# Performance work log

Measured on AMD Instinct MI355X. Metric: run time of the kernel, lower is better.

Reference implementation:

```python
import jax, jax.numpy as jnp
import numpy as np

N = 50000
E = 800000
IN_DIM = 128
HIDDEN = 32
HEADS = 4
OUT_DIM = 64
NEG_SLOPE = 0.2


def _glorot(key, shape):
    fan_in, fan_out = shape[0], shape[-1]
    lim = jnp.sqrt(6.0 / (fan_in + fan_out))
    return jax.random.uniform(key, shape, jnp.float32, -lim, lim)


def setup_inputs() -> dict:
    key = jax.random.key(0)
    ks = jax.random.split(key, 16)
    x = jax.random.normal(ks[0], (N, IN_DIM), jnp.float32)
    edge_index = jax.random.randint(ks[1], (2, E), 0, N, jnp.int64)
    # layer 0: in_dim -> hidden, heads, concat
    W1 = _glorot(ks[2], (IN_DIM, HEADS * HIDDEN))
    a_src1 = _glorot(ks[3], (HEADS, HIDDEN))
    a_dst1 = _glorot(ks[4], (HEADS, HIDDEN))
    b1 = jnp.zeros((HEADS * HIDDEN,), jnp.float32)
    # layer 1: hidden*heads -> hidden, heads, concat
    W2 = _glorot(ks[5], (HEADS * HIDDEN, HEADS * HIDDEN))
    a_src2 = _glorot(ks[6], (HEADS, HIDDEN))
    a_dst2 = _glorot(ks[7], (HEADS, HIDDEN))
    b2 = jnp.zeros((HEADS * HIDDEN,), jnp.float32)
    # layer 2: hidden*heads -> out_dim, heads, concat=False (mean over heads)
    W3 = _glorot(ks[8], (HEADS * HIDDEN, HEADS * OUT_DIM))
    a_src3 = _glorot(ks[9], (HEADS, OUT_DIM))
    a_dst3 = _glorot(ks[10], (HEADS, OUT_DIM))
    b3 = jnp.zeros((OUT_DIM,), jnp.float32)
    return {"x": x, "edge_index": edge_index,
            "W1": W1, "a_src1": a_src1, "a_dst1": a_dst1, "b1": b1,
            "W2": W2, "a_src2": a_src2, "a_dst2": a_dst2, "b2": b2,
            "W3": W3, "a_src3": a_src3, "a_dst3": a_dst3, "b3": b3}


def gat_conv(x, src, dst, W, a_src, a_dst, bias, out_ch, concat):
    # linear projection, per-head view: [N, H, C]
    h = (x @ W).reshape(N, HEADS, out_ch)
    # per-node attention logits, gathered to edges: [E, H]
    alpha_src = jnp.einsum('nhc,hc->nh', h, a_src)
    alpha_dst = jnp.einsum('nhc,hc->nh', h, a_dst)
    e = jax.nn.leaky_relu(alpha_src[src] + alpha_dst[dst], NEG_SLOPE)
    # segment softmax over incoming edges of each dst node
    m = jax.ops.segment_max(e, dst, num_segments=N)  # [N, H]
    m = jnp.where(jnp.isfinite(m), m, 0.0)
    p = jnp.exp(e - m[dst])  # [E, H]
    denom = jax.ops.segment_sum(p, dst, num_segments=N)  # [N, H]
    alpha = p / (denom[dst] + 1e-16)
    # weighted scatter-add of source features: [N, H, C]
    out = jax.ops.segment_sum(h[src] * alpha[:, :, None], dst, num_segments=N)
    if concat:
        return out.reshape(N, HEADS * out_ch) + bias
    return out.mean(axis=1) + bias


def reference(x, edge_index, W1, a_src1, a_dst1, b1, W2, a_src2, a_dst2, b2,
              W3, a_src3, a_dst3, b3):
    src, dst = edge_index[0], edge_index[1]
    x = gat_conv(x, src, dst, W1, a_src1, a_dst1, b1, HIDDEN, True)
    x = gat_conv(x, src, dst, W2, a_src2, a_dst2, b2, HIDDEN, True)
    x = gat_conv(x, src, dst, W3, a_src3, a_dst3, b3, OUT_DIM, False)
    return x
```

## Files before the change

### kernel.cpp

```cpp
#include <hip/hip_runtime.h>
#include <hip/hip_fp16.h>
#include <math.h>

#define NNODES 50000
#define NEDGES 800000

typedef _Float16 half8 __attribute__((ext_vector_type(8)));
typedef float floatx4 __attribute__((ext_vector_type(4)));


__global__ void zero_i32(int* __restrict__ p, int n) {
    int i = blockIdx.x * 256 + threadIdx.x;
    if (i < n) p[i] = 0;
}

__global__ void hist_kernel(const int* __restrict__ dst, int* __restrict__ counts, int e) {
    int i = blockIdx.x * 256 + threadIdx.x;
    if (i < e) atomicAdd(&counts[dst[i]], 1);
}

__global__ void scan1_kernel(const int* __restrict__ counts, int* __restrict__ row_ptr,
                             int* __restrict__ bsums, int n) {
    __shared__ int s[256];
    int tid = threadIdx.x;
    int i = blockIdx.x * 256 + tid;
    int v = (i < n) ? counts[i] : 0;
    s[tid] = v;
    __syncthreads();
    #pragma unroll
    for (int o = 1; o < 256; o <<= 1) {
        int t = (tid >= o) ? s[tid - o] : 0;
        __syncthreads();
        s[tid] += t;
        __syncthreads();
    }
    if (i < n) row_ptr[i + 1] = s[tid];
    if (tid == 255) bsums[blockIdx.x] = s[255];
}

__global__ void scan2_kernel(int* __restrict__ bsums, int nb) {
    __shared__ int s[256];
    int tid = threadIdx.x;
    int v = (tid < nb) ? bsums[tid] : 0;
    s[tid] = v;
    __syncthreads();
    #pragma unroll
    for (int o = 1; o < 256; o <<= 1) {
        int t = (tid >= o) ? s[tid - o] : 0;
        __syncthreads();
        s[tid] += t;
        __syncthreads();
    }
    if (tid < nb) bsums[tid] = s[tid] - v;
}

__global__ void scan3_kernel(int* __restrict__ row_ptr, const int* __restrict__ bsums,
                             int* __restrict__ cursor, int n) {
    int i = blockIdx.x * 256 + threadIdx.x;
    if (i < n) {
        row_ptr[i + 1] += bsums[blockIdx.x];
        cursor[i] = 0;
    }
    if (i == 0) row_ptr[0] = 0;
}

__global__ void fill_kernel(const int* __restrict__ src, const int* __restrict__ dst,
                            const int* __restrict__ row_ptr, int* __restrict__ cursor,
                            int* __restrict__ csr_src, int e) {
    int i = blockIdx.x * 256 + threadIdx.x;
    if (i < e) {
        int d = dst[i];
        int pos = atomicAdd(&cursor[d], 1);
        csr_src[row_ptr[d] + pos] = src[i];
    }
}

__global__ void prep_v_kernel(const float* __restrict__ W3, const float* __restrict__ as3,
                              const float* __restrict__ ad3, float* __restrict__ Vs,
                              float* __restrict__ Vd) {
    int id = blockIdx.x * 256 + threadIdx.x;
    if (id >= 1024) return;
    int which = id >> 9;
    int rem = id & 511;
    int k = rem >> 2;
    int hd = rem & 3;
    const float* av = which ? ad3 : as3;
    float s = 0.f;
    #pragma unroll 8
    for (int c = 0; c < 64; ++c)
        s += W3[(size_t)k * 256 + hd * 64 + c] * av[hd * 64 + c];
    (which ? Vd : Vs)[hd * 128 + k] = s;
}

__global__ void prep_wr_kernel(const float* __restrict__ W3, __half* __restrict__ Wr) {
    int id = blockIdx.x * 256 + threadIdx.x;
    if (id >= 64 * 512) return;
    int c = id >> 9;
    int rem = id & 511;
    int hd = rem >> 7;
    int k = rem & 127;
    Wr[(size_t)c * 512 + hd * 128 + k] = __float2half(W3[(size_t)k * 256 + hd * 64 + c]);
}

__global__ __launch_bounds__(256) void alpha3_kernel(const __half* __restrict__ A,
                                                     const float* __restrict__ Vs,
                                                     const float* __restrict__ Vd,
                                                     float* __restrict__ asrc,
                                                     float* __restrict__ adst, int n) {
    int wid = threadIdx.x >> 6;
    int lane = threadIdx.x & 63;
    int node = blockIdx.x * 4 + wid;
    if (node >= n) return;
    unsigned raw = *(const unsigned*)(A + (size_t)node * 128 + lane * 2);
    float2 f = __half22float2(*(const __half2*)&raw);
    float ss[4], sd[4];
    #pragma unroll
    for (int hd = 0; hd < 4; ++hd) {
        ss[hd] = f.x * Vs[hd * 128 + lane * 2] + f.y * Vs[hd * 128 + lane * 2 + 1];
        sd[hd] = f.x * Vd[hd * 128 + lane * 2] + f.y * Vd[hd * 128 + lane * 2 + 1];
    }
    #pragma unroll
    for (int o = 1; o < 64; o <<= 1) {
        #pragma unroll
        for (int hd = 0; hd < 4; ++hd) {
            ss[hd] += __shfl_xor(ss[hd], o);
            sd[hd] += __shfl_xor(sd[hd], o);
        }
    }
    if (lane == 0) {
        #pragma unroll
        for (int hd = 0; hd < 4; ++hd) {
            asrc[(size_t)node * 4 + hd] = ss[hd];
            adst[(size_t)node * 4 + hd] = sd[hd];
        }
    }
}


template <bool AF32, int LAYER>
__global__ __launch_bounds__(256, 3) void gemm_mfma(const void* __restrict__ A_,
                                                    const float* __restrict__ Wf,
                                                    const float* __restrict__ a_src,
                                                    const float* __restrict__ a_dst,
                                                    __half* __restrict__ H,
                                                    float* __restrict__ asrc,
                                                    float* __restrict__ adst, int n) {
    const int M = 128, CH = 32;
    __shared__ __half As[128][136];
    __shared__ __half Ws[64][136];
    int tid = threadIdx.x;
    int row0 = blockIdx.x * 128;
    int col0 = blockIdx.y * 64;

    if constexpr (AF32) {
        const float* Af = (const float*)A_;
        #pragma unroll
        for (int it = 0; it < 8; ++it) {
            int flat = tid + it * 256;
            int r = flat >> 4;
            int kq = (flat & 15) * 8;
            int gr = row0 + r;
            float4 v0 = {0.f, 0.f, 0.f, 0.f}, v1 = {0.f, 0.f, 0.f, 0.f};
            if (gr < n) {
                v0 = *(const float4*)&Af[(size_t)gr * 128 + kq];
                v1 = *(const float4*)&Af[(size_t)gr * 128 + kq + 4];
            }
            __half2 h0 = __floats2half2_rn(v0.x, v0.y);
            __half2 h1 = __floats2half2_rn(v0.z, v0.w);
            __half2 h2 = __floats2half2_rn(v1.x, v1.y);
            __half2 h3 = __floats2half2_rn(v1.z, v1.w);
            uint4 st = {*(unsigned*)&h0, *(unsigned*)&h1, *(unsigned*)&h2, *(unsigned*)&h3};
            *(uint4*)&As[r][kq] = st;
        }
    } else {
        const __half* Ah = (const __half*)A_;
        #pragma unroll
        for (int it = 0; it < 8; ++it) {
            int flat = tid + it * 256;
            int r = flat >> 4;
            int kq = (flat & 15) * 8;
            int gr = row0 + r;
            float4 v = {0.f, 0.f, 0.f, 0.f};
            if (gr < n) v = *(const float4*)&Ah[(size_t)gr * 128 + kq];
            *(float4*)&As[r][kq] = v;
        }
    }
    #pragma unroll
    for (int it = 0; it < 4; ++it) {
        int flat = tid + it * 256;
        int kp = flat >> 4;
        int c4 = (flat & 15) * 4;
        int k = kp * 2;
        float4 va = *(const float4*)&Wf[(size_t)k * M + col0 + c4];
        float4 vb = *(const float4*)&Wf[(size_t)(k + 1) * M + col0 + c4];
        *(__half2*)&Ws[c4 + 0][k] = __floats2half2_rn(va.x, vb.x);
        *(__half2*)&Ws[c4 + 1][k] = __floats2half2_rn(va.y, vb.y);
        *(__half2*)&Ws[c4 + 2][k] = __floats2half2_rn(va.z, vb.z);
        *(__half2*)&Ws[c4 + 3][k] = __floats2half2_rn(va.w, vb.w);
    }
    __syncthreads();

    int lane = tid & 63;
    int wid = tid >> 6;
    int wm = (wid >> 1) * 64;
    int wn = (wid & 1) * 32;
    int l15 = lane & 15;
    int l4 = lane >> 4;

    floatx4 acc[4][2];
    #pragma unroll
    for (int mf = 0; mf < 4; ++mf)
        #pragma unroll
        for (int nf = 0; nf < 2; ++nf) {
            floatx4 z = {0.f, 0.f, 0.f, 0.f};
            acc[mf][nf] = z;
        }

    #pragma unroll
    for (int ks = 0; ks < 4; ++ks) {
        int kb = ks * 32 + l4 * 8;
        half8 b0 = *(const half8*)&Ws[wn + l15][kb];
        half8 b1 = *(const half8*)&Ws[wn + 16 + l15][kb];
        #pragma unroll
        for (int mf = 0; mf < 4; ++mf) {
            half8 a = *(const half8*)&As[wm + mf * 16 + l15][kb];
            acc[mf][0] = __builtin_amdgcn_mfma_f32_16x16x32_f16(a, b0, acc[mf][0], 0, 0, 0);
            acc[mf][1] = __builtin_amdgcn_mfma_f32_16x16x32_f16(a, b1, acc[mf][1], 0, 0, 0);
        }
    }

    #pragma unroll
    for (int mf = 0; mf < 4; ++mf)
        #pragma unroll
        for (int r = 0; r < 4; ++r) {
            int gr = row0 + wm + mf * 16 + l4 * 4 + r;
            if (gr < n) {
                H[(size_t)gr * M + col0 + wn + l15] = __float2half(acc[mf][0][r]);
                H[(size_t)gr * M + col0 + wn + 16 + l15] = __float2half(acc[mf][1][r]);
            }
        }

    int hw = (col0 + wn) / CH;
    float vs0 = a_src[hw * CH + l15];
    float vs1 = a_src[hw * CH + 16 + l15];
    float vd0 = a_dst[hw * CH + l15];
    float vd1 = a_dst[hw * CH + 16 + l15];

    #pragma unroll
    for (int mf = 0; mf < 4; ++mf)
        #pragma unroll
        for (int r = 0; r < 4; ++r) {
            float ss = acc[mf][0][r] * vs0 + acc[mf][1][r] * vs1;
            float sd = acc[mf][0][r] * vd0 + acc[mf][1][r] * vd1;
            #pragma unroll
            for (int o = 1; o < 16; o <<= 1) {
                ss += __shfl_xor(ss, o);
                sd += __shfl_xor(sd, o);
            }
            int gr = row0 + wm + mf * 16 + l4 * 4 + r;
            if (l15 == 0 && gr < n) {
                asrc[(size_t)gr * 4 + hw] = ss;
                adst[(size_t)gr * 4 + hw] = sd;
            }
        }
}


template <int LAYER>
__global__ __launch_bounds__(256) void aggregate_kernel(
    const __half* __restrict__ h, const float* __restrict__ asrc,
    const float* __restrict__ adst, const int* __restrict__ csr_src,
    const int* __restrict__ row_ptr, const float* __restrict__ bias,
    __half* __restrict__ out, int n) {
    __shared__ float lds[4][332];
    int wid = threadIdx.x >> 6;
    int lane = threadIdx.x & 63;
    int node = blockIdx.x * 4 + wid;
    if (node >= n) return;
    float* Wp = lds[wid];
    int* Ws = (int*)&lds[wid][264];
    int start = row_ptr[node];
    int end = row_ptr[node + 1];
    float4 ad = *(const float4*)&adst[(size_t)node * 4];

    int l32 = lane & 31, head = l32 >> 3, j_off = lane >> 5;
    int hoff = head * 66;

    float acc0 = 0.f, acc1 = 0.f, acc2 = 0.f, acc3 = 0.f, pw = 0.f;

    for (int base = start; base < end; base += 64) {
        int cnt = end - base;
        if (cnt > 64) cnt = 64;
        int s = 0;
        float4 pv = {0.f, 0.f, 0.f, 0.f};
        if (lane < cnt) {
            s = csr_src[base + lane];
            float4 a = *(const float4*)&asrc[(size_t)s * 4];
            float e0 = a.x + ad.x; e0 = (e0 > 0.f) ? e0 : 0.2f * e0;
            float e1 = a.y + ad.y; e1 = (e1 > 0.f) ? e1 : 0.2f * e1;
            float e2 = a.z + ad.z; e2 = (e2 > 0.f) ? e2 : 0.2f * e2;
            float e3 = a.w + ad.w; e3 = (e3 > 0.f) ? e3 : 0.2f * e3;
            pv.x = __expf(e0); pv.y = __expf(e1); pv.z = __expf(e2); pv.w = __expf(e3);
        }
        Wp[0 * 66 + lane] = pv.x;
        Wp[1 * 66 + lane] = pv.y;
        Wp[2 * 66 + lane] = pv.z;
        Wp[3 * 66 + lane] = pv.w;
        Ws[lane] = s;
        __builtin_amdgcn_wave_barrier();
        asm volatile("" ::: "memory");
        for (int jj = 0; jj < cnt; jj += 16) {
            float w[8]; int sa[8];
            #pragma unroll
            for (int u = 0; u < 8; ++u) {
                int j = jj + 2 * u + j_off;
                w[u] = Wp[hoff + j];
                sa[u] = Ws[j];
            }
            float2 v[8];
            #pragma unroll
            for (int u = 0; u < 8; ++u)
                v[u] = *(const float2*)(h + (size_t)sa[u] * 128 + l32 * 4);
            #pragma unroll
            for (int u = 0; u < 8; ++u) {
                float2 f01 = __half22float2(((const __half2*)&v[u])[0]);
                float2 f23 = __half22float2(((const __half2*)&v[u])[1]);
                acc0 += w[u] * f01.x;
                acc1 += w[u] * f01.y;
                acc2 += w[u] * f23.x;
                acc3 += w[u] * f23.y;
                pw += w[u];
            }
        }
        __builtin_amdgcn_wave_barrier();
        asm volatile("" ::: "memory");
    }

    acc0 += __shfl_xor(acc0, 32);
    acc1 += __shfl_xor(acc1, 32);
    acc2 += __shfl_xor(acc2, 32);
    acc3 += __shfl_xor(acc3, 32);
    pw += __shfl_xor(pw, 32);
    if (lane < 32) {
        float inv = 1.f / (pw + 1e-16f);
        float4 b = *(const float4*)&bias[l32 * 4];
        __half2 ha = __floats2half2_rn(acc0 * inv + b.x, acc1 * inv + b.y);
        __half2 hb = __floats2half2_rn(acc2 * inv + b.z, acc3 * inv + b.w);
        uint2 st = {*(unsigned int*)&ha, *(unsigned int*)&hb};
        *(uint2*)&out[(size_t)node * 128 + l32 * 4] = st;
    }
}


__global__ __launch_bounds__(256) void aggregate_x_kernel(
    const __half* __restrict__ A, const float* __restrict__ asrc,
    const float* __restrict__ adst, const int* __restrict__ csr_src,
    const int* __restrict__ row_ptr, __half* __restrict__ S, int n) {
    __shared__ float lds[4][320];
    int wid = threadIdx.x >> 6;
    int lane = threadIdx.x & 63;
    int node = blockIdx.x * 4 + wid;
    if (node >= n) return;
    float* Wp4 = lds[wid];
    int* Ws = (int*)&lds[wid][256];
    int start = row_ptr[node];
    int end = row_ptr[node + 1];
    float4 ad = *(const float4*)&adst[(size_t)node * 4];

    float a00 = 0.f, a01 = 0.f, a10 = 0.f, a11 = 0.f;
    float a20 = 0.f, a21 = 0.f, a30 = 0.f, a31 = 0.f;
    float4 psum = {0.f, 0.f, 0.f, 0.f};

    for (int base = start; base < end; base += 64) {
        int cnt = end - base;
        if (cnt > 64) cnt = 64;
        int s = 0;
        float4 pv = {0.f, 0.f, 0.f, 0.f};
        if (lane < cnt) {
            s = csr_src[base + lane];
            float4 a = *(const float4*)&asrc[(size_t)s * 4];
            float e0 = a.x + ad.x; e0 = (e0 > 0.f) ? e0 : 0.2f * e0;
            float e1 = a.y + ad.y; e1 = (e1 > 0.f) ? e1 : 0.2f * e1;
            float e2 = a.z + ad.z; e2 = (e2 > 0.f) ? e2 : 0.2f * e2;
            float e3 = a.w + ad.w; e3 = (e3 > 0.f) ? e3 : 0.2f * e3;
            pv.x = __expf(e0); pv.y = __expf(e1); pv.z = __expf(e2); pv.w = __expf(e3);
            psum.x += pv.x; psum.y += pv.y; psum.z += pv.z; psum.w += pv.w;
        }
        *(float4*)&Wp4[lane * 4] = pv;
        Ws[lane] = s;
        __builtin_amdgcn_wave_barrier();
        asm volatile("" ::: "memory");
        for (int jj = 0; jj < cnt; jj += 8) {
            int sa[8];
            #pragma unroll
            for (int u = 0; u < 8; ++u) sa[u] = Ws[jj + u];
            unsigned raw[8];
            #pragma unroll
            for (int u = 0; u < 8; ++u)
                raw[u] = *(const unsigned*)(A + (size_t)sa[u] * 128 + lane * 2);
            #pragma unroll
            for (int u = 0; u < 8; ++u) {
                float4 p = *(const float4*)&Wp4[(jj + u) * 4];
                float2 f = __half22float2(*(const __half2*)&raw[u]);
                a00 += p.x * f.x; a01 += p.x * f.y;
                a10 += p.y * f.x; a11 += p.y * f.y;
                a20 += p.z * f.x; a21 += p.z * f.y;
                a30 += p.w * f.x; a31 += p.w * f.y;
            }
        }
        __builtin_amdgcn_wave_barrier();
        asm volatile("" ::: "memory");
    }

    #pragma unroll
    for (int o = 1; o < 64; o <<= 1) {
        psum.x += __shfl_xor(psum.x, o);
        psum.y += __shfl_xor(psum.y, o);
        psum.z += __shfl_xor(psum.z, o);
        psum.w += __shfl_xor(psum.w, o);
    }
    float s0 = 0.25f / (psum.x + 1e-16f);
    float s1 = 0.25f / (psum.y + 1e-16f);
    float s2 = 0.25f / (psum.z + 1e-16f);
    float s3 = 0.25f / (psum.w + 1e-16f);
    size_t sb = (size_t)node * 512 + lane * 2;
    *(__half2*)&S[sb + 0 * 128] = __floats2half2_rn(a00 * s0, a01 * s0);
    *(__half2*)&S[sb + 1 * 128] = __floats2half2_rn(a10 * s1, a11 * s1);
    *(__half2*)&S[sb + 2 * 128] = __floats2half2_rn(a20 * s2, a21 * s2);
    *(__half2*)&S[sb + 3 * 128] = __floats2half2_rn(a30 * s3, a31 * s3);
}


__global__ __launch_bounds__(256, 3) void post_gemm(const __half* __restrict__ S,
                                                    const __half* __restrict__ Wr,
                                                    const float* __restrict__ b3,
                                                    float* __restrict__ out, int n) {
    __shared__ __half As[128][136];
    __shared__ __half Ws[64][136];
    int tid = threadIdx.x;
    int row0 = blockIdx.x * 128;
    int lane = tid & 63;
    int wid = tid >> 6;
    int wm = (wid >> 1) * 64;
    int wn = (wid & 1) * 32;
    int l15 = lane & 15;
    int l4 = lane >> 4;

    floatx4 acc[4][2];
    #pragma unroll
    for (int mf = 0; mf < 4; ++mf)
        #pragma unroll
        for (int nf = 0; nf < 2; ++nf) {
            floatx4 z = {0.f, 0.f, 0.f, 0.f};
            acc[mf][nf] = z;
        }

    for (int kb = 0; kb < 512; kb += 128) {
        #pragma unroll
        for (int it = 0; it < 8; ++it) {
            int flat = tid + it * 256;
            int r = flat >> 4;
            int kq = (flat & 15) * 8;
            int gr = row0 + r;
            float4 v = {0.f, 0.f, 0.f, 0.f};
            if (gr < n) v = *(const float4*)&S[(size_t)gr * 512 + kb + kq];
            *(float4*)&As[r][kq] = v;
        }
        #pragma unroll
        for (int it = 0; it < 4; ++it) {
            int flat = tid + it * 256;
            int r = flat >> 4;
            int kq = (flat & 15) * 8;
            *(float4*)&Ws[r][kq] = *(const float4*)&Wr[(size_t)r * 512 + kb + kq];
        }
        __syncthreads();
        #pragma unroll
        for (int ks = 0; ks < 4; ++ks) {
            int kk = ks * 32 + l4 * 8;
            half8 b0 = *(const half8*)&Ws[wn + l15][kk];
            half8 b1 = *(const half8*)&Ws[wn + 16 + l15][kk];
            #pragma unroll
            for (int mf = 0; mf < 4; ++mf) {
                half8 a = *(const half8*)&As[wm + mf * 16 + l15][kk];
                acc[mf][0] = __builtin_amdgcn_mfma_f32_16x16x32_f16(a, b0, acc[mf][0], 0, 0, 0);
                acc[mf][1] = __builtin_amdgcn_mfma_f32_16x16x32_f16(a, b1, acc[mf][1], 0, 0, 0);
            }
        }
        __syncthreads();
    }

    float bl = b3[wn + l15];
    float bh = b3[wn + 16 + l15];
    #pragma unroll
    for (int mf = 0; mf < 4; ++mf)
        #pragma unroll
        for (int r = 0; r < 4; ++r) {
            int gr = row0 + wm + mf * 16 + l4 * 4 + r;
            if (gr < n) {
                out[(size_t)gr * 64 + wn + l15] = acc[mf][0][r] + bl;
                out[(size_t)gr * 64 + wn + 16 + l15] = acc[mf][1][r] + bh;
            }
        }
}


extern "C" void kernel_launch(void* const* d_in, const int* in_sizes, int n_in,
                              void* d_out, int out_size, void* d_ws, size_t ws_size,
                              hipStream_t stream) {
    const float* x = (const float*)d_in[0];
    const int* ei = (const int*)d_in[1];
    const int* src = ei;
    const int* dst = ei + NEDGES;
    const float* W1 = (const float*)d_in[2];
    const float* as1 = (const float*)d_in[3];
    const float* ad1 = (const float*)d_in[4];
    const float* b1 = (const float*)d_in[5];
    const float* W2 = (const float*)d_in[6];
    const float* as2 = (const float*)d_in[7];
    const float* ad2 = (const float*)d_in[8];
    const float* b2 = (const float*)d_in[9];
    const float* W3 = (const float*)d_in[10];
    const float* as3 = (const float*)d_in[11];
    const float* ad3 = (const float*)d_in[12];
    const float* b3 = (const float*)d_in[13];

    char* ws = (char*)d_ws;
    size_t off = 0;
    auto take = [&](size_t bytes) -> char* {
        char* p = ws + off;
        off = (off + bytes + 255) & ~(size_t)255;
        return p;
    };
    int* csr = (int*)take((size_t)NEDGES * 4);
    int* row_ptr = (int*)take((size_t)(NNODES + 1) * 4);
    int* counts = (int*)take((size_t)NNODES * 4);
    int* cursor = (int*)take((size_t)NNODES * 4);
    int* bsums = (int*)take(1024 * 4);
    float* asrc = (float*)take((size_t)NNODES * 4 * 4);
    float* adst = (float*)take((size_t)NNODES * 4 * 4);
    __half* hbuf = (__half*)take((size_t)NNODES * 128 * 2);
    __half* buf1h = (__half*)take((size_t)NNODES * 128 * 2);
    __half* Sbuf = (__half*)take((size_t)NNODES * 512 * 2);
    float* Vs = (float*)take(512 * 4);
    float* Vd = (float*)take(512 * 4);
    __half* Wr = (__half*)take((size_t)64 * 512 * 2);
    float* outp = (float*)d_out;

    int nbN = (NNODES + 255) / 256;
    int nbE = (NEDGES + 255) / 256;
    int gnodeAgg = (NNODES + 3) / 4;

    zero_i32<<<nbN, 256, 0, stream>>>(counts, NNODES);
    hist_kernel<<<nbE, 256, 0, stream>>>(dst, counts, NEDGES);
    scan1_kernel<<<nbN, 256, 0, stream>>>(counts, row_ptr, bsums, NNODES);
    scan2_kernel<<<1, 256, 0, stream>>>(bsums, nbN);
    scan3_kernel<<<nbN, 256, 0, stream>>>(row_ptr, bsums, cursor, NNODES);
    fill_kernel<<<nbE, 256, 0, stream>>>(src, dst, row_ptr, cursor, csr, NEDGES);
    prep_v_kernel<<<4, 256, 0, stream>>>(W3, as3, ad3, Vs, Vd);
    prep_wr_kernel<<<128, 256, 0, stream>>>(W3, Wr);

    dim3 gA((NNODES + 127) / 128, 2);

    gemm_mfma<true, 1><<<gA, 256, 0, stream>>>(x, W1, as1, ad1, hbuf, asrc, adst, NNODES);
    aggregate_kernel<1><<<gnodeAgg, 256, 0, stream>>>(hbuf, asrc, adst, csr, row_ptr, b1, buf1h, NNODES);

    gemm_mfma<false, 2><<<gA, 256, 0, stream>>>(buf1h, W2, as2, ad2, hbuf, asrc, adst, NNODES);
    aggregate_kernel<2><<<gnodeAgg, 256, 0, stream>>>(hbuf, asrc, adst, csr, row_ptr, b2, buf1h, NNODES);

    alpha3_kernel<<<gnodeAgg, 256, 0, stream>>>(buf1h, Vs, Vd, asrc, adst, NNODES);
    aggregate_x_kernel<<<gnodeAgg, 256, 0, stream>>>(buf1h, asrc, adst, csr, row_ptr, Sbuf, NNODES);
    post_gemm<<<(NNODES + 127) / 128, 256, 0, stream>>>(Sbuf, Wr, b3, outp, NNODES);
}
```

Baseline: 297.1 us.

## Fuse layer-3 attention logits into layer-2 aggregation and remap lanes per channel

Removes the separate alpha3 kernel by computing the layer-3 source and destination logits inside the layer-2 aggregation epilogue, using the freshly computed outputs still in registers. To support this, the aggregation is remapped so each of the 64 lanes owns two channels across all edges, not half the edges with four channels each. The per-edge weights are now stored as a float4 per edge in LDS, and the final cross-half shuffle reduction goes away. Separate asrc3/adst3 buffers avoid overwriting the logits still being read. The trade-off is that each edge gather is now a 4-byte load per lane instead of 8 bytes, with twice as many inner iterations per edge chunk.

```diff
diff --git a/kernel.cpp b/kernel.cpp
--- a/kernel.cpp
+++ b/kernel.cpp
@@ -102,40 +102,6 @@
     Wr[(size_t)c * 512 + hd * 128 + k] = __float2half(W3[(size_t)k * 256 + hd * 64 + c]);
 }
 
-__global__ __launch_bounds__(256) void alpha3_kernel(const __half* __restrict__ A,
-                                                     const float* __restrict__ Vs,
-                                                     const float* __restrict__ Vd,
-                                                     float* __restrict__ asrc,
-                                                     float* __restrict__ adst, int n) {
-    int wid = threadIdx.x >> 6;
-    int lane = threadIdx.x & 63;
-    int node = blockIdx.x * 4 + wid;
-    if (node >= n) return;
-    unsigned raw = *(const unsigned*)(A + (size_t)node * 128 + lane * 2);
-    float2 f = __half22float2(*(const __half2*)&raw);
-    float ss[4], sd[4];
-    #pragma unroll
-    for (int hd = 0; hd < 4; ++hd) {
-        ss[hd] = f.x * Vs[hd * 128 + lane * 2] + f.y * Vs[hd * 128 + lane * 2 + 1];
-        sd[hd] = f.x * Vd[hd * 128 + lane * 2] + f.y * Vd[hd * 128 + lane * 2 + 1];
-    }
-    #pragma unroll
-    for (int o = 1; o < 64; o <<= 1) {
-        #pragma unroll
-        for (int hd = 0; hd < 4; ++hd) {
-            ss[hd] += __shfl_xor(ss[hd], o);
-            sd[hd] += __shfl_xor(sd[hd], o);
-        }
-    }
-    if (lane == 0) {
-        #pragma unroll
-        for (int hd = 0; hd < 4; ++hd) {
-            asrc[(size_t)node * 4 + hd] = ss[hd];
-            adst[(size_t)node * 4 + hd] = sd[hd];
-        }
-    }
-}
-
 
 template <bool AF32, int LAYER>
 __global__ __launch_bounds__(256, 3) void gemm_mfma(const void* __restrict__ A_,
@@ -266,27 +232,27 @@
 }
 
 
-template <int LAYER>
+template <int LAYER, bool FUSE_A3>
 __global__ __launch_bounds__(256) void aggregate_kernel(
     const __half* __restrict__ h, const float* __restrict__ asrc,
     const float* __restrict__ adst, const int* __restrict__ csr_src,
     const int* __restrict__ row_ptr, const float* __restrict__ bias,
-    __half* __restrict__ out, int n) {
-    __shared__ float lds[4][332];
+    const float* __restrict__ Vs, const float* __restrict__ Vd,
+    __half* __restrict__ out, float* __restrict__ asrc3,
+    float* __restrict__ adst3, int n) {
+    __shared__ float lds[4][320];
     int wid = threadIdx.x >> 6;
     int lane = threadIdx.x & 63;
     int node = blockIdx.x * 4 + wid;
     if (node >= n) return;
-    float* Wp = lds[wid];
-    int* Ws = (int*)&lds[wid][264];
+    float* Wp4 = lds[wid];
+    int* Ws = (int*)&lds[wid][256];
     int start = row_ptr[node];
     int end = row_ptr[node + 1];
     float4 ad = *(const float4*)&adst[(size_t)node * 4];
-
-    int l32 = lane & 31, head = l32 >> 3, j_off = lane >> 5;
-    int hoff = head * 66;
-
-    float acc0 = 0.f, acc1 = 0.f, acc2 = 0.f, acc3 = 0.f, pw = 0.f;
+    int head = lane >> 4;
+
+    float acc0 = 0.f, acc1 = 0.f, pw = 0.f;
 
     for (int base = start; base < end; base += 64) {
         int cnt = end - base;
@@ -302,33 +268,26 @@
             float e3 = a.w + ad.w; e3 = (e3 > 0.f) ? e3 : 0.2f * e3;
             pv.x = __expf(e0); pv.y = __expf(e1); pv.z = __expf(e2); pv.w = __expf(e3);
         }
-        Wp[0 * 66 + lane] = pv.x;
-        Wp[1 * 66 + lane] = pv.y;
-        Wp[2 * 66 + lane] = pv.z;
-        Wp[3 * 66 + lane] = pv.w;
+        *(float4*)&Wp4[lane * 4] = pv;
         Ws[lane] = s;
         __builtin_amdgcn_wave_barrier();
         asm volatile("" ::: "memory");
-        for (int jj = 0; jj < cnt; jj += 16) {
+        for (int jj = 0; jj < cnt; jj += 8) {
             float w[8]; int sa[8];
             #pragma unroll
             for (int u = 0; u < 8; ++u) {
-                int j = jj + 2 * u + j_off;
-                w[u] = Wp[hoff + j];
-                sa[u] = Ws[j];
-            }
-            float2 v[8];
+                w[u] = Wp4[(jj + u) * 4 + head];
+                sa[u] = Ws[jj + u];
+            }
+            unsigned raw[8];
             #pragma unroll
             for (int u = 0; u < 8; ++u)
-                v[u] = *(const float2*)(h + (size_t)sa[u] * 128 + l32 * 4);
+                raw[u] = *(const unsigned*)(h + (size_t)sa[u] * 128 + lane * 2);
             #pragma unroll
             for (int u = 0; u < 8; ++u) {
-                float2 f01 = __half22float2(((const __half2*)&v[u])[0]);
-                float2 f23 = __half22float2(((const __half2*)&v[u])[1]);
-                acc0 += w[u] * f01.x;
-                acc1 += w[u] * f01.y;
-                acc2 += w[u] * f23.x;
-                acc3 += w[u] * f23.y;
+                float2 f = __half22float2(*(const __half2*)&raw[u]);
+                acc0 += w[u] * f.x;
+                acc1 += w[u] * f.y;
                 pw += w[u];
             }
         }
@@ -336,18 +295,31 @@
         asm volatile("" ::: "memory");
     }
 
-    acc0 += __shfl_xor(acc0, 32);
-    acc1 += __shfl_xor(acc1, 32);
-    acc2 += __shfl_xor(acc2, 32);
-    acc3 += __shfl_xor(acc3, 32);
-    pw += __shfl_xor(pw, 32);
-    if (lane < 32) {
-        float inv = 1.f / (pw + 1e-16f);
-        float4 b = *(const float4*)&bias[l32 * 4];
-        __half2 ha = __floats2half2_rn(acc0 * inv + b.x, acc1 * inv + b.y);
-        __half2 hb = __floats2half2_rn(acc2 * inv + b.z, acc3 * inv + b.w);
-        uint2 st = {*(unsigned int*)&ha, *(unsigned int*)&hb};
-        *(uint2*)&out[(size_t)node * 128 + l32 * 4] = st;
+    float inv = 1.f / (pw + 1e-16f);
+    float2 b = *(const float2*)&bias[lane * 2];
+    float o0 = acc0 * inv + b.x;
+    float o1 = acc1 * inv + b.y;
+    *(__half2*)&out[(size_t)node * 128 + lane * 2] = __floats2half2_rn(o0, o1);
+
+    if constexpr (FUSE_A3) {
+        float r[8];
+        #pragma unroll
+        for (int hd = 0; hd < 4; ++hd) {
+            r[hd]     = o0 * Vs[hd * 128 + lane * 2] + o1 * Vs[hd * 128 + lane * 2 + 1];
+            r[hd + 4] = o0 * Vd[hd * 128 + lane * 2] + o1 * Vd[hd * 128 + lane * 2 + 1];
+        }
+        #pragma unroll
+        for (int o = 1; o < 64; o <<= 1) {
+            #pragma unroll
+            for (int q = 0; q < 8; ++q) r[q] += __shfl_xor(r[q], o);
+        }
+        if (lane == 0) {
+            #pragma unroll
+            for (int hd = 0; hd < 4; ++hd) {
+                asrc3[(size_t)node * 4 + hd] = r[hd];
+                adst3[(size_t)node * 4 + hd] = r[hd + 4];
+            }
+        }
     }
 }
 
@@ -538,6 +510,8 @@
     int* bsums = (int*)take(1024 * 4);
     float* asrc = (float*)take((size_t)NNODES * 4 * 4);
     float* adst = (float*)take((size_t)NNODES * 4 * 4);
+    float* asrc3 = (float*)take((size_t)NNODES * 4 * 4);
+    float* adst3 = (float*)take((size_t)NNODES * 4 * 4);
     __half* hbuf = (__half*)take((size_t)NNODES * 128 * 2);
     __half* buf1h = (__half*)take((size_t)NNODES * 128 * 2);
     __half* Sbuf = (__half*)take((size_t)NNODES * 512 * 2);
@@ -562,12 +536,13 @@
     dim3 gA((NNODES + 127) / 128, 2);
 
     gemm_mfma<true, 1><<<gA, 256, 0, stream>>>(x, W1, as1, ad1, hbuf, asrc, adst, NNODES);
-    aggregate_kernel<1><<<gnodeAgg, 256, 0, stream>>>(hbuf, asrc, adst, csr, row_ptr, b1, buf1h, NNODES);
+    aggregate_kernel<1, false><<<gnodeAgg, 256, 0, stream>>>(
+        hbuf, asrc, adst, csr, row_ptr, b1, nullptr, nullptr, buf1h, nullptr, nullptr, NNODES);
 
     gemm_mfma<false, 2><<<gA, 256, 0, stream>>>(buf1h, W2, as2, ad2, hbuf, asrc, adst, NNODES);
-    aggregate_kernel<2><<<gnodeAgg, 256, 0, stream>>>(hbuf, asrc, adst, csr, row_ptr, b2, buf1h, NNODES);
-
-    alpha3_kernel<<<gnodeAgg, 256, 0, stream>>>(buf1h, Vs, Vd, asrc, adst, NNODES);
-    aggregate_x_kernel<<<gnodeAgg, 256, 0, stream>>>(buf1h, asrc, adst, csr, row_ptr, Sbuf, NNODES);
+    aggregate_kernel<2, true><<<gnodeAgg, 256, 0, stream>>>(
+        hbuf, asrc, adst, csr, row_ptr, b2, Vs, Vd, buf1h, asrc3, adst3, NNODES);
+
+    aggregate_x_kernel<<<gnodeAgg, 256, 0, stream>>>(buf1h, asrc3, adst3, csr, row_ptr, Sbuf, NNODES);
     post_gemm<<<(NNODES + 127) / 128, 256, 0, stream>>>(Sbuf, Wr, b3, outp, NNODES);
 }
```

Result: faster. 281.6 us (-5.2%).
